# Performance work log

Hardware: AMD Instinct MI355X
Metric: run time of the kernel (lower is better)

The kernel has to match this reference:

```python
import jax, jax.numpy as jnp
import numpy as np
import math

B, L, IN_F, OUT_F = 16, 4096, 384, 384
SCALE = 1.0 / math.sqrt(IN_F)
EPS = 1e-8


def setup_inputs() -> dict:
    key = jax.random.key(0)
    k1, k2, k3 = jax.random.split(key, 3)
    return {
        "Efou": jax.random.normal(k1, (B, L, IN_F), dtype=jnp.float32),
        "y": jax.random.normal(k2, (B, IN_F), dtype=jnp.float32),
        "weight": jax.random.normal(k3, (1, OUT_F, IN_F), dtype=jnp.float32),
    }


def reference(Efou, y, weight):
    b, size_patch, in_f = Efou.shape
    out_f = weight.shape[1]
    # per-sample weight modulation: [B, out, in]
    w = SCALE * weight * y[:, None, :]
    # demodulation
    dconf = jax.lax.rsqrt(jnp.sum(w * w, axis=2) + EPS)  # [B, out]
    w = w * dconf[:, :, None]
    # Faithful raw reshape of [B, L, in] buffer to [B, in, L] layout (NOT a transpose),
    # matching torch's Efou.reshape(1, B*in, L) + grouped conv1d with kernel size 1.
    Xr = Efou.reshape(b, in_f, size_patch)
    out = jnp.einsum("boi,bip->bop", w, Xr)  # [B, out, L]
    # Faithful raw view of (B*out, L) buffer as (B, L, out)
    return out.reshape(b, size_patch, out_f)
```

## Files before the change

kernel.cpp:

```cpp
#include <hip/hip_runtime.h>
#include <hip/hip_bf16.h>
#include <stdint.h>

#define Bn 16
#define Ln 4096
#define KF 384
#define OF 384

#define BM 128
#define BN 128
#define BK 64
#define LDX 72

static constexpr float kScale = 0.051031036307982884f;

typedef __attribute__((ext_vector_type(4))) float f32x4;
typedef __attribute__((ext_vector_type(2))) float f32x2;
typedef __attribute__((ext_vector_type(8))) short short8;
typedef __attribute__((ext_vector_type(4))) float floatx4;
typedef __attribute__((ext_vector_type(4))) unsigned int uint4v;

__device__ __forceinline__ void gl_lds16(const void* g, void* l) {
  __builtin_amdgcn_global_load_lds(
      (const __attribute__((address_space(1))) unsigned int*)g,
      (__attribute__((address_space(3))) unsigned int*)l, 16, 0, 0);
}

__device__ __forceinline__ unsigned int f2bf_bits(float f) {
  union { float f; unsigned int u; } v;
  v.f = f;
  return (v.u + 0x7FFFu + ((v.u >> 16) & 1u)) >> 16;
}
__device__ __forceinline__ unsigned int pack2bf(float lo, float hi) {
  return f2bf_bits(lo) | (f2bf_bits(hi) << 16);
}

__device__ __forceinline__ unsigned int cvt_pk_bf16(float lo, float hi) {
  unsigned int r;
  asm("v_cvt_pk_bf16_f32 %0, %1, %2" : "=v"(r) : "v"(lo), "v"(hi));
  return r;
}

__global__ __launch_bounds__(256) void modw_kernel(const float* __restrict__ weight,
                                                   const float* __restrict__ y,
                                                   unsigned short* __restrict__ wmod) {
  int t = threadIdx.x;
  int wv = t >> 6, lane = t & 63;
  int row = blockIdx.x * 4 + wv;
  int b = row / OF, o = row % OF;
  const float* wr = weight + o * KF;
  const float* yr = y + b * KF;
  float vals[6];
  float ss = 0.f;
#pragma unroll
  for (int j = 0; j < 3; ++j) {
    int k = (lane + 64 * j) * 2;
    f32x2 wvv = *(const f32x2*)(wr + k);
    f32x2 yv = *(const f32x2*)(yr + k);
    float t0 = kScale * wvv[0] * yv[0];
    float t1 = kScale * wvv[1] * yv[1];
    vals[2 * j] = t0;
    vals[2 * j + 1] = t1;
    ss += t0 * t0 + t1 * t1;
  }
#pragma unroll
  for (int off = 32; off >= 1; off >>= 1) ss += __shfl_xor(ss, off, 64);
  float d = rsqrtf(ss + 1e-8f);
  unsigned short* orow = wmod + row * KF;
#pragma unroll
  for (int j = 0; j < 3; ++j) {
    int k = (lane + 64 * j) * 2;
    *(unsigned int*)(orow + k) = pack2bf(vals[2 * j] * d, vals[2 * j + 1] * d);
  }
}

__global__ __launch_bounds__(256, 3) void gemm_kernel(const float* __restrict__ X,
                                                      const unsigned short* __restrict__ Wm,
                                                      float* __restrict__ out) {
  __shared__ unsigned short sA[2][BM * BK];
  __shared__ unsigned short sX[2][BN * LDX];

  int flat = blockIdx.x;
  int logical = (flat & 7) * 192 + (flat >> 3);
  int mt = logical % 3;
  int nt = (logical / 3) & 31;
  int b = logical / 96;

  int t = threadIdx.x;
  int wave = t >> 6, lane = t & 63;
  int quad = lane >> 4;

  const float* Xb = X + b * (KF * Ln);
  const unsigned short* Wb = Wm + (b * OF + mt * BM) * KF;
  int pbase = nt * BN;

  floatx4 acc[4][4] = {};

  int i31 = t & 31;
  int p0 = i31 * 4;
  int kr0 = (t >> 5) * 8;
  int kr0s = (((t >> 5) ^ (i31 & 7)) * 8);
  int arow = (wave >> 1) * 64 + (lane & 15);
  int brow = (wave & 1) * 64 + (lane & 15);
  int asw = lane & 7;
  int xsw = ((lane & 15) >> 2);

  int aoff[4], asrc_row[4], asrc_c[4];
#pragma unroll
  for (int j = 0; j < 4; ++j) {
    int boff = wave * 4096 + j * 1024 + lane * 16;
    int row = boff >> 7;
    int cp = (boff >> 4) & 7;
    aoff[j] = boff;
    asrc_row[j] = row;
    asrc_c[j] = (cp ^ (row & 7)) * 8;
  }

  f32x4 xv[8];
  unsigned int wv4[4][4];

#pragma unroll
  for (int j = 0; j < 4; ++j)
    gl_lds16(Wb + asrc_row[j] * KF + 0 + asrc_c[j], (char*)sA[0] + aoff[j]);
  {
    const float* xsrc = Xb + (0 + kr0) * Ln + pbase + p0;
#pragma unroll
    for (int i = 0; i < 8; ++i) xv[i] = *(const f32x4*)(xsrc + i * Ln);
#pragma unroll
    for (int j = 0; j < 4; ++j)
#pragma unroll
      for (int i = 0; i < 4; ++i)
        wv4[j][i] = cvt_pk_bf16(xv[2 * i][j], xv[2 * i + 1][j]);
#pragma unroll
    for (int j = 0; j < 4; ++j)
      *(uint4v*)(&sX[0][(p0 + j) * LDX + kr0s]) = *(uint4v*)wv4[j];
  }
  {
    const float* xsrc = Xb + (BK + kr0) * Ln + pbase + p0;
#pragma unroll
    for (int i = 0; i < 8; ++i) xv[i] = *(const f32x4*)(xsrc + i * Ln);
  }
  asm volatile("s_waitcnt lgkmcnt(0)" ::: "memory");
  __builtin_amdgcn_sched_barrier(0);
  __builtin_amdgcn_s_barrier();

#pragma unroll
  for (int kc = 0; kc < 6; ++kc) {
    int cur = kc & 1;
    if (kc < 5) {
      int k0n = (kc + 1) * BK;
#pragma unroll
      for (int j = 0; j < 4; ++j)
        gl_lds16(Wb + asrc_row[j] * KF + k0n + asrc_c[j], (char*)sA[cur ^ 1] + aoff[j]);
    }
#pragma unroll
    for (int s = 0; s < 2; ++s) {
      short8 af[4], bf[4];
#pragma unroll
      for (int mi = 0; mi < 4; ++mi) {
        int ca = (((s << 2) | quad) ^ asw) * 8;
        af[mi] = *(const short8*)(&sA[cur][(arow + mi * 16) * BK + ca]);
      }
#pragma unroll
      for (int ni = 0; ni < 4; ++ni) {
        int cx = (((s << 2) | quad) ^ (((ni & 1) << 2) | xsw)) * 8;
        bf[ni] = *(const short8*)(&sX[cur][(brow + ni * 16) * LDX + cx]);
      }
      __builtin_amdgcn_s_setprio(1);
#pragma unroll
      for (int mi = 0; mi < 4; ++mi)
#pragma unroll
        for (int ni = 0; ni < 4; ++ni)
          acc[mi][ni] = __builtin_amdgcn_mfma_f32_16x16x32_bf16(af[mi], bf[ni], acc[mi][ni], 0, 0, 0);
      __builtin_amdgcn_s_setprio(0);
    }
    if (kc < 5) {
#pragma unroll
      for (int j = 0; j < 4; ++j)
#pragma unroll
        for (int i = 0; i < 4; ++i)
          wv4[j][i] = cvt_pk_bf16(xv[2 * i][j], xv[2 * i + 1][j]);
#pragma unroll
      for (int j = 0; j < 4; ++j)
        *(uint4v*)(&sX[cur ^ 1][(p0 + j) * LDX + kr0s]) = *(uint4v*)wv4[j];
      if (kc < 4) {
        const float* xsrc = Xb + ((kc + 2) * BK + kr0) * Ln + pbase + p0;
#pragma unroll
        for (int i = 0; i < 8; ++i) xv[i] = *(const f32x4*)(xsrc + i * Ln);
      }
      if (kc < 4) {
        asm volatile("s_waitcnt vmcnt(8)" ::: "memory");
      } else {
        asm volatile("s_waitcnt vmcnt(0)" ::: "memory");
      }
      asm volatile("s_waitcnt lgkmcnt(0)" ::: "memory");
      __builtin_amdgcn_sched_barrier(0);
      __builtin_amdgcn_s_barrier();
    }
  }

  float* outb = out + (b * OF + mt * BM) * Ln + pbase;
  int col = lane & 15;
#pragma unroll
  for (int mi = 0; mi < 4; ++mi) {
    int ob = (wave >> 1) * 64 + mi * 16 + quad * 4;
#pragma unroll
    for (int ni = 0; ni < 4; ++ni) {
      int p = (wave & 1) * 64 + ni * 16 + col;
#pragma unroll
      for (int r = 0; r < 4; ++r) outb[(ob + r) * Ln + p] = acc[mi][ni][r];
    }
  }
}

extern "C" void kernel_launch(void* const* d_in, const int* in_sizes, int n_in,
                              void* d_out, int out_size, void* d_ws, size_t ws_size,
                              hipStream_t stream) {
  const float* Efou = (const float*)d_in[0];
  const float* y = (const float*)d_in[1];
  const float* weight = (const float*)d_in[2];
  float* out = (float*)d_out;
  unsigned short* wmod = (unsigned short*)d_ws;

  modw_kernel<<<(Bn * OF) / 4, 256, 0, stream>>>(weight, y, wmod);
  gemm_kernel<<<Bn * (OF / BM) * (Ln / BN), 256, 0, stream>>>(Efou, wmod, out);
}
```

Before: 198.7 us.

## Halve N tile, single-buffer weight tile, and raise occupancy to four blocks

Shrinks the GEMM N tile from 128 to 64 columns, so each block's accumulators and X staging registers are halved. The weight tile in LDS goes from double to single buffering, with an extra barrier before it is reloaded. Launch bounds rise to 4 blocks per CU and the grid remapping doubles to match. The goal is higher occupancy to hide memory latency, at the cost of less reuse per block (each weight tile is loaded twice as often), an extra barrier per K step, and weight loads no longer overlapping the MFMA work.

```diff
diff --git a/kernel.cpp b/kernel.cpp
--- a/kernel.cpp
+++ b/kernel.cpp
@@ -8,7 +8,7 @@
 #define OF 384
 
 #define BM 128
-#define BN 128
+#define BN 64
 #define BK 64
 #define LDX 72
 
@@ -18,7 +18,7 @@
 typedef __attribute__((ext_vector_type(2))) float f32x2;
 typedef __attribute__((ext_vector_type(8))) short short8;
 typedef __attribute__((ext_vector_type(4))) float floatx4;
-typedef __attribute__((ext_vector_type(4))) unsigned int uint4v;
+typedef __attribute__((ext_vector_type(2))) unsigned int uint2v;
 
 __device__ __forceinline__ void gl_lds16(const void* g, void* l) {
   __builtin_amdgcn_global_load_lds(
@@ -74,36 +74,35 @@
   }
 }
 
-__global__ __launch_bounds__(256, 3) void gemm_kernel(const float* __restrict__ X,
+__global__ __launch_bounds__(256, 4) void gemm_kernel(const float* __restrict__ X,
                                                       const unsigned short* __restrict__ Wm,
                                                       float* __restrict__ out) {
-  __shared__ unsigned short sA[2][BM * BK];
+  __shared__ unsigned short sA[BM * BK];
   __shared__ unsigned short sX[2][BN * LDX];
 
   int flat = blockIdx.x;
-  int logical = (flat & 7) * 192 + (flat >> 3);
+  int logical = (flat & 7) * 384 + (flat >> 3);
   int mt = logical % 3;
-  int nt = (logical / 3) & 31;
-  int b = logical / 96;
+  int nt = (logical / 3) & 63;
+  int b = logical / 192;
 
   int t = threadIdx.x;
   int wave = t >> 6, lane = t & 63;
-  int quad = lane >> 4;
+  int quad = lane >> 4, l15 = lane & 15;
 
   const float* Xb = X + b * (KF * Ln);
   const unsigned short* Wb = Wm + (b * OF + mt * BM) * KF;
   int pbase = nt * BN;
 
-  floatx4 acc[4][4] = {};
-
-  int i31 = t & 31;
-  int p0 = i31 * 4;
-  int kr0 = (t >> 5) * 8;
-  int kr0s = (((t >> 5) ^ (i31 & 7)) * 8);
-  int arow = (wave >> 1) * 64 + (lane & 15);
-  int brow = (wave & 1) * 64 + (lane & 15);
+  floatx4 acc[4][2] = {};
+
+  int p0 = (t & 15) * 4;
+  int kr0 = (t >> 4) * 4;
+  int swk = (((kr0 >> 3) ^ (t & 7)) * 8) + (kr0 & 4);
+  int arow = (wave >> 1) * 64 + l15;
+  int brow = (wave & 1) * 32 + l15;
   int asw = lane & 7;
-  int xsw = ((lane & 15) >> 2);
+  int xsw = l15 >> 2;
 
   int aoff[4], asrc_row[4], asrc_c[4];
 #pragma unroll
@@ -116,29 +115,29 @@
     asrc_c[j] = (cp ^ (row & 7)) * 8;
   }
 
-  f32x4 xv[8];
-  unsigned int wv4[4][4];
+  f32x4 xv[4];
+  uint2v wv[4];
 
 #pragma unroll
   for (int j = 0; j < 4; ++j)
-    gl_lds16(Wb + asrc_row[j] * KF + 0 + asrc_c[j], (char*)sA[0] + aoff[j]);
+    gl_lds16(Wb + asrc_row[j] * KF + 0 + asrc_c[j], (char*)sA + aoff[j]);
   {
-    const float* xsrc = Xb + (0 + kr0) * Ln + pbase + p0;
-#pragma unroll
-    for (int i = 0; i < 8; ++i) xv[i] = *(const f32x4*)(xsrc + i * Ln);
+    const float* xsrc = Xb + kr0 * Ln + pbase + p0;
+#pragma unroll
+    for (int i = 0; i < 4; ++i) xv[i] = *(const f32x4*)(xsrc + i * Ln);
+#pragma unroll
+    for (int j = 0; j < 4; ++j) {
+      wv[j][0] = cvt_pk_bf16(xv[0][j], xv[1][j]);
+      wv[j][1] = cvt_pk_bf16(xv[2][j], xv[3][j]);
+    }
 #pragma unroll
     for (int j = 0; j < 4; ++j)
-#pragma unroll
-      for (int i = 0; i < 4; ++i)
-        wv4[j][i] = cvt_pk_bf16(xv[2 * i][j], xv[2 * i + 1][j]);
-#pragma unroll
-    for (int j = 0; j < 4; ++j)
-      *(uint4v*)(&sX[0][(p0 + j) * LDX + kr0s]) = *(uint4v*)wv4[j];
+      *(uint2v*)(&sX[0][(p0 + j) * LDX + swk]) = wv[j];
   }
   {
     const float* xsrc = Xb + (BK + kr0) * Ln + pbase + p0;
 #pragma unroll
-    for (int i = 0; i < 8; ++i) xv[i] = *(const f32x4*)(xsrc + i * Ln);
+    for (int i = 0; i < 4; ++i) xv[i] = *(const f32x4*)(xsrc + i * Ln);
   }
   asm volatile("s_waitcnt lgkmcnt(0)" ::: "memory");
   __builtin_amdgcn_sched_barrier(0);
@@ -147,49 +146,48 @@
 #pragma unroll
   for (int kc = 0; kc < 6; ++kc) {
     int cur = kc & 1;
-    if (kc < 5) {
-      int k0n = (kc + 1) * BK;
-#pragma unroll
-      for (int j = 0; j < 4; ++j)
-        gl_lds16(Wb + asrc_row[j] * KF + k0n + asrc_c[j], (char*)sA[cur ^ 1] + aoff[j]);
-    }
 #pragma unroll
     for (int s = 0; s < 2; ++s) {
-      short8 af[4], bf[4];
+      short8 af[4], bfr[2];
 #pragma unroll
       for (int mi = 0; mi < 4; ++mi) {
         int ca = (((s << 2) | quad) ^ asw) * 8;
-        af[mi] = *(const short8*)(&sA[cur][(arow + mi * 16) * BK + ca]);
-      }
-#pragma unroll
-      for (int ni = 0; ni < 4; ++ni) {
-        int cx = (((s << 2) | quad) ^ (((ni & 1) << 2) | xsw)) * 8;
-        bf[ni] = *(const short8*)(&sX[cur][(brow + ni * 16) * LDX + cx]);
+        af[mi] = *(const short8*)(&sA[(arow + mi * 16) * BK + ca]);
+      }
+#pragma unroll
+      for (int ni = 0; ni < 2; ++ni) {
+        int cx = (((s << 2) | quad) ^ ((ni << 2) | xsw)) * 8;
+        bfr[ni] = *(const short8*)(&sX[cur][(brow + ni * 16) * LDX + cx]);
       }
       __builtin_amdgcn_s_setprio(1);
 #pragma unroll
       for (int mi = 0; mi < 4; ++mi)
 #pragma unroll
-        for (int ni = 0; ni < 4; ++ni)
-          acc[mi][ni] = __builtin_amdgcn_mfma_f32_16x16x32_bf16(af[mi], bf[ni], acc[mi][ni], 0, 0, 0);
+        for (int ni = 0; ni < 2; ++ni)
+          acc[mi][ni] = __builtin_amdgcn_mfma_f32_16x16x32_bf16(af[mi], bfr[ni], acc[mi][ni], 0, 0, 0);
       __builtin_amdgcn_s_setprio(0);
     }
     if (kc < 5) {
 #pragma unroll
+      for (int j = 0; j < 4; ++j) {
+        wv[j][0] = cvt_pk_bf16(xv[0][j], xv[1][j]);
+        wv[j][1] = cvt_pk_bf16(xv[2][j], xv[3][j]);
+      }
+      __builtin_amdgcn_sched_barrier(0);
+      __builtin_amdgcn_s_barrier();
+      __builtin_amdgcn_sched_barrier(0);
+      int k0n = (kc + 1) * BK;
+#pragma unroll
       for (int j = 0; j < 4; ++j)
-#pragma unroll
-        for (int i = 0; i < 4; ++i)
-          wv4[j][i] = cvt_pk_bf16(xv[2 * i][j], xv[2 * i + 1][j]);
+        gl_lds16(Wb + asrc_row[j] * KF + k0n + asrc_c[j], (char*)sA + aoff[j]);
 #pragma unroll
       for (int j = 0; j < 4; ++j)
-        *(uint4v*)(&sX[cur ^ 1][(p0 + j) * LDX + kr0s]) = *(uint4v*)wv4[j];
+        *(uint2v*)(&sX[cur ^ 1][(p0 + j) * LDX + swk]) = wv[j];
       if (kc < 4) {
         const float* xsrc = Xb + ((kc + 2) * BK + kr0) * Ln + pbase + p0;
 #pragma unroll
-        for (int i = 0; i < 8; ++i) xv[i] = *(const f32x4*)(xsrc + i * Ln);
-      }
-      if (kc < 4) {
-        asm volatile("s_waitcnt vmcnt(8)" ::: "memory");
+        for (int i = 0; i < 4; ++i) xv[i] = *(const f32x4*)(xsrc + i * Ln);
+        asm volatile("s_waitcnt vmcnt(4)" ::: "memory");
       } else {
         asm volatile("s_waitcnt vmcnt(0)" ::: "memory");
       }
@@ -200,13 +198,12 @@
   }
 
   float* outb = out + (b * OF + mt * BM) * Ln + pbase;
-  int col = lane & 15;
 #pragma unroll
   for (int mi = 0; mi < 4; ++mi) {
     int ob = (wave >> 1) * 64 + mi * 16 + quad * 4;
 #pragma unroll
-    for (int ni = 0; ni < 4; ++ni) {
-      int p = (wave & 1) * 64 + ni * 16 + col;
+    for (int ni = 0; ni < 2; ++ni) {
+      int p = (wave & 1) * 32 + ni * 16 + l15;
 #pragma unroll
       for (int r = 0; r < 4; ++r) outb[(ob + r) * Ln + p] = acc[mi][ni][r];
     }
```

Result: slower. 203.1 us (+2.2%).
